# Performance work log

Hardware: AMD Instinct MI355X
Metric: run time of the kernel (lower is better)

Reference implementation:

```python
import jax, jax.numpy as jnp
import numpy as np

B, V, J, NS, NE = 2048, 5023, 5, 100, 50
PB = 9 * (J - 1)  # pose basis = 36


def setup_inputs() -> dict:
    key = jax.random.key(0)
    ks = jax.random.split(key, 8)
    jr = jax.random.uniform(ks[5], (J, V), dtype=jnp.float32)
    lw = jax.random.uniform(ks[6], (V, J), dtype=jnp.float32)
    return {
        "shape_params": jax.random.normal(ks[0], (B, NS), dtype=jnp.float32),
        "expression_params": jax.random.normal(ks[1], (B, NE), dtype=jnp.float32),
        "pose": jax.random.normal(ks[2], (B, J * 3), dtype=jnp.float32) * 0.2,
        "v_template": jax.random.normal(ks[3], (V, 3), dtype=jnp.float32) * 0.1,
        "shapedirs": jax.random.normal(ks[4], (V, 3, NS + NE), dtype=jnp.float32) * 0.01,
        "posedirs": jax.random.normal(ks[7], (PB, V * 3), dtype=jnp.float32) * 0.01,
        "J_regressor": jr / jnp.sum(jr, axis=1, keepdims=True),   # rows sum to 1 (convex combos)
        "lbs_weights": lw / jnp.sum(lw, axis=1, keepdims=True),   # rows sum to 1 (skinning weights)
        "parents": np.array([0, 0, 1, 1, 1], dtype=np.int64),     # FLAME kintree (root entry unused)
    }


def batch_rodrigues(rot_vecs):
    """(N,3) axis-angle -> (N,3,3) rotation matrices (matches torch ref incl. +1e-8)."""
    angle = jnp.linalg.norm(rot_vecs + 1e-8, axis=1, keepdims=True)      # (N,1)
    rd = rot_vecs / angle
    cos = jnp.cos(angle)[:, :, None]                                      # (N,1,1)
    sin = jnp.sin(angle)[:, :, None]
    rx, ry, rz = rd[:, 0], rd[:, 1], rd[:, 2]
    z = jnp.zeros_like(rx)
    K = jnp.stack([z, -rz, ry, rz, z, -rx, -ry, rx, z], axis=1).reshape(-1, 3, 3)
    I = jnp.eye(3, dtype=rot_vecs.dtype)
    return I + sin * K + (1.0 - cos) * jnp.matmul(K, K)


def reference(shape_params, expression_params, pose, v_template, shapedirs,
              posedirs, J_regressor, lbs_weights, parents):
    par = np.asarray(parents)  # static kinematic tree
    b = shape_params.shape[0]
    betas = jnp.concatenate([shape_params, expression_params], axis=1)     # (B,150)
    v_shaped = v_template + jnp.einsum('bl,vkl->bvk', betas, shapedirs)    # (B,V,3)
    Jts = jnp.einsum('bvk,jv->bjk', v_shaped, J_regressor)                 # (B,J,3)
    # pose -> rotations, pose-corrective offsets
    rot_mats = batch_rodrigues(pose.reshape(-1, 3)).reshape(b, -1, 3, 3)   # (B,J,3,3)
    I3 = jnp.eye(3, dtype=pose.dtype)
    pose_feature = (rot_mats[:, 1:] - I3).reshape(b, -1)                   # (B,36)
    pose_offsets = jnp.matmul(pose_feature, posedirs).reshape(b, -1, 3)    # (B,V,3)
    v_posed = v_posed = pose_offsets + v_shaped
    # kinematic chain (relative joint transforms -> world transforms)
    rel_joints = jnp.concatenate(
        [Jts[:, :1], Jts[:, 1:] - Jts[:, par[1:]]], axis=1)                # (B,J,3)
    top = jnp.concatenate([rot_mats, rel_joints[..., None]], axis=-1)      # (B,J,3,4)
    bottom = jnp.broadcast_to(
        jnp.array([0., 0., 0., 1.], dtype=pose.dtype), (b, Jts.shape[1], 1, 4))
    tm = jnp.concatenate([top, bottom], axis=2)                            # (B,J,4,4)
    chain = [tm[:, 0]]
    for i in range(1, par.shape[0]):  # tiny fixed loop over 5 joints
        chain.append(jnp.matmul(chain[int(par[i])], tm[:, i]))
    transforms = jnp.stack(chain, axis=1)                                  # (B,J,4,4)
    posed_joints = transforms[:, :, :3, 3]
    # remove rest-pose joint locations: subtract (transforms @ [j;0]) from last column
    tj = jnp.einsum('bjmn,bjn->bjm', transforms[:, :, :, :3], Jts)         # (B,J,4)
    rel_transforms = transforms.at[:, :, :, 3].add(-tj)                    # (B,J,4,4)
    # linear blend skinning
    T = jnp.einsum('vj,bjmn->bvmn', lbs_weights, rel_transforms)           # (B,V,4,4)
    verts = jnp.einsum('bvmn,bvn->bvm', T[:, :, :3, :3], v_posed) + T[:, :, :3, 3]
    return verts, posed_joints
```

## Files before the change

kernel.cpp:

```cpp
#include <hip/hip_runtime.h>
#include <hip/hip_bf16.h>
#include <math.h>

#define B_N 2048
#define V_N 5023
#define V3_N 15069
#define NSJB 157
#define CHUNK 32

typedef float f32x4 __attribute__((ext_vector_type(4)));
typedef short short8 __attribute__((ext_vector_type(8)));

static __device__ __forceinline__ ushort f2bf(float f) {
  __hip_bfloat16 h = __float2bfloat16(f);
  return *reinterpret_cast<ushort*>(&h);
}

__global__ void k_zero(float* __restrict__ SJ) {
  int id = blockIdx.x * 256 + threadIdx.x;
  if (id < 2280) SJ[id] = 0.0f;
}

__global__ __launch_bounds__(256) void k_pre(const float* __restrict__ sdirs,
                                             const float* __restrict__ pdirs,
                                             const float* __restrict__ vtemp,
                                             const float* __restrict__ Jr,
                                             const float* __restrict__ shp,
                                             const float* __restrict__ expr,
                                             ushort* __restrict__ basis,
                                             float* __restrict__ SJ,
                                             ushort* __restrict__ bb) {
  __shared__ float Sh[16][452];
  __shared__ float Pd[36][48];
  int t = threadIdx.x, blk = blockIdx.x;
  if (blk < 314) {
    int bx = blk, v0 = bx * 16;
    for (int idx = t; idx < 16 * 450; idx += 256) {
      int r = idx / 450, c = idx - r * 450;
      int v = v0 + r;
      Sh[r][c] = (v < V_N) ? sdirs[(size_t)v * 450 + c] : 0.0f;
    }
    for (int idx = t; idx < 36 * 48; idx += 256) {
      int p = idx / 48, c = idx - p * 48;
      int v3 = v0 * 3 + c;
      Pd[p][c] = (v3 < V3_N) ? pdirs[(size_t)p * V3_N + v3] : 0.0f;
    }
    __syncthreads();
    for (int idx = t; idx < 64 * 96; idx += 256) {
      int row = idx / 96, kp = idx - row * 96;
      int vl = row >> 2, c = row & 3;
      int k0 = kp * 2;
      float f0 = 0.0f, f1 = 0.0f;
      if (c < 3) {
        if (k0 < 150) {
          f0 = Sh[vl][c * 150 + k0];
          f1 = Sh[vl][c * 150 + k0 + 1];
        } else if (k0 < 186) {
          f0 = Pd[k0 - 150][vl * 3 + c];
          f1 = Pd[k0 - 149][vl * 3 + c];
        }
      }
      uint u = (uint)f2bf(f0) | ((uint)f2bf(f1) << 16);
      int kb = kp >> 2, e = kp & 3;
      ((uint*)basis)[(size_t)(bx * 64 + row) * 96 + (((kb ^ (row & 7)) << 2) + e)] = u;
    }
  } else if (blk < 314 + NSJB) {
    float (*JrL)[CHUNK] = (float(*)[CHUNK]) & Sh[0][0];
    int bk = blk - 314;
    int vstart = bk * CHUNK;
    int cnt = min(CHUNK, V_N - vstart);
    for (int idx = t; idx < 5 * CHUNK; idx += 256) {
      int j = idx / CHUNK, vi = idx % CHUNK;
      JrL[j][vi] = (vi < cnt) ? Jr[j * V_N + vstart + vi] : 0.0f;
    }
    __syncthreads();
    float acc0[5] = {0, 0, 0, 0, 0}, acc1[5] = {0, 0, 0, 0, 0};
    int c0 = t, c1 = t + 256;
#pragma unroll 4
    for (int vi = 0; vi < CHUNK; ++vi) {
      int v = min(vstart + vi, V_N - 1);
      float val0 = sdirs[(size_t)v * 450 + c0];
      float val1 = 0.0f;
      if (c1 < 450) val1 = sdirs[(size_t)v * 450 + c1];
      else if (c1 < 453) val1 = vtemp[(size_t)v * 3 + (c1 - 450)];
#pragma unroll
      for (int j = 0; j < 5; ++j) {
        float w = JrL[j][vi];
        acc0[j] = fmaf(w, val0, acc0[j]);
        acc1[j] = fmaf(w, val1, acc1[j]);
      }
    }
#pragma unroll
    for (int j = 0; j < 5; ++j) {
      atomicAdd(&SJ[j * 456 + c0], acc0[j]);
      if (c1 < 453) atomicAdd(&SJ[j * 456 + c1], acc1[j]);
    }
  } else {
    int idx = (blk - 314 - NSJB) * 256 + t;
    int b = idx / 96, cp = idx - b * 96;
    int c0 = cp * 2;
    float f0 = 0.0f, f1 = 0.0f;
    if (c0 < 100) {
      f0 = shp[(size_t)b * 100 + c0];
      f1 = shp[(size_t)b * 100 + c0 + 1];
    } else if (c0 < 150) {
      f0 = expr[(size_t)b * 50 + (c0 - 100)];
      f1 = expr[(size_t)b * 50 + (c0 - 99)];
    }
    int r = b & 63;
    int kb = cp >> 2, e = cp & 3;
    ((uint*)bb)[(size_t)b * 96 + (((kb ^ (r & 7)) << 2) + e)] =
        (uint)f2bf(f0) | ((uint)f2bf(f1) << 16);
  }
}

__global__ __launch_bounds__(256) void k_jpose(const float* __restrict__ shp,
                                               const float* __restrict__ expr,
                                               const float* __restrict__ SJ,
                                               const float* __restrict__ pose,
                                               ushort* __restrict__ bb,
                                               float* __restrict__ A,
                                               float* __restrict__ out) {
  __shared__ float JtL[16][16];
  int t = threadIdx.x;
  int g = t >> 4, r = t & 15;
  int b = blockIdx.x * 16 + g;
  if (r < 15) {
    int j = r / 3, k = r - j * 3;
    const float* SJr = SJ + j * 456;
    float acc = SJr[450 + k];
    const float* srow = shp + (size_t)b * 100;
    const float* erow = expr + (size_t)b * 50;
    for (int l = 0; l < 100; ++l) acc = fmaf(srow[l], SJr[k * 150 + l], acc);
    for (int l = 0; l < 50; ++l) acc = fmaf(erow[l], SJr[k * 150 + 100 + l], acc);
    JtL[g][r] = acc;
  }
  __syncthreads();
  if (r != 0) return;
  float R[5][3][3];
#pragma unroll
  for (int j = 0; j < 5; ++j) {
    float rx = pose[(size_t)b * 15 + j * 3 + 0];
    float ry = pose[(size_t)b * 15 + j * 3 + 1];
    float rz = pose[(size_t)b * 15 + j * 3 + 2];
    float sx = rx + 1e-8f, sy = ry + 1e-8f, sz = rz + 1e-8f;
    float ang = sqrtf(sx * sx + sy * sy + sz * sz);
    float inv = 1.0f / ang;
    float ux = rx * inv, uy = ry * inv, uz = rz * inv;
    float c = cosf(ang), s = sinf(ang), omc = 1.0f - c;
    float K[3][3] = {{0.0f, -uz, uy}, {uz, 0.0f, -ux}, {-uy, ux, 0.0f}};
#pragma unroll
    for (int m = 0; m < 3; ++m)
#pragma unroll
      for (int n = 0; n < 3; ++n) {
        float k2 = 0.0f;
#pragma unroll
        for (int q = 0; q < 3; ++q) k2 += K[m][q] * K[q][n];
        R[j][m][n] = ((m == n) ? 1.0f : 0.0f) + s * K[m][n] + omc * k2;
      }
  }
  {
    float pf[36];
#pragma unroll
    for (int j = 1; j < 5; ++j)
#pragma unroll
      for (int m = 0; m < 3; ++m)
#pragma unroll
        for (int n = 0; n < 3; ++n)
          pf[(j - 1) * 9 + m * 3 + n] = R[j][m][n] - ((m == n) ? 1.0f : 0.0f);
    uint* bbu = (uint*)bb + (size_t)b * 96;
    int rr = b & 7;
#pragma unroll
    for (int q = 0; q < 18; ++q) {
      int cp = 75 + q;
      int kb = cp >> 2, e = cp & 3;
      bbu[((kb ^ rr) << 2) + e] = (uint)f2bf(pf[2 * q]) | ((uint)f2bf(pf[2 * q + 1]) << 16);
    }
  }
  float Jt[5][3];
#pragma unroll
  for (int j = 0; j < 5; ++j)
#pragma unroll
    for (int k = 0; k < 3; ++k) Jt[j][k] = JtL[g][j * 3 + k];
  const int par[5] = {0, 0, 1, 1, 1};
  float rel[5][3];
#pragma unroll
  for (int k = 0; k < 3; ++k) rel[0][k] = Jt[0][k];
#pragma unroll
  for (int j = 1; j < 5; ++j)
#pragma unroll
    for (int k = 0; k < 3; ++k) rel[j][k] = Jt[j][k] - Jt[par[j]][k];
  float Rg[5][3][3], tg[5][3];
#pragma unroll
  for (int m = 0; m < 3; ++m) {
#pragma unroll
    for (int n = 0; n < 3; ++n) Rg[0][m][n] = R[0][m][n];
    tg[0][m] = rel[0][m];
  }
#pragma unroll
  for (int j = 1; j < 5; ++j) {
    int p = par[j];
#pragma unroll
    for (int m = 0; m < 3; ++m) {
      float t2 = tg[p][m];
#pragma unroll
      for (int n = 0; n < 3; ++n) {
        float s = 0.0f;
#pragma unroll
        for (int q = 0; q < 3; ++q) s = fmaf(Rg[p][m][q], R[j][q][n], s);
        Rg[j][m][n] = s;
        t2 = fmaf(Rg[p][m][n], rel[j][n], t2);
      }
      tg[j][m] = t2;
    }
  }
#pragma unroll
  for (int j = 0; j < 5; ++j)
#pragma unroll
    for (int k = 0; k < 3; ++k)
      out[(size_t)B_N * V_N * 3 + ((size_t)b * 5 + j) * 3 + k] = tg[j][k];
  float Af[5][12];
#pragma unroll
  for (int j = 0; j < 5; ++j)
#pragma unroll
    for (int m = 0; m < 3; ++m) {
      float tj = 0.0f;
#pragma unroll
      for (int n = 0; n < 3; ++n) {
        Af[j][m * 4 + n] = Rg[j][m][n];
        tj = fmaf(Rg[j][m][n], Jt[j][n], tj);
      }
      Af[j][m * 4 + 3] = tg[j][m] - tj;
    }
  float* Ab = A + (size_t)b * 64;
#pragma unroll
  for (int q = 0; q < 12; ++q) Ab[q] = Af[0][q];
#pragma unroll
  for (int j = 1; j < 5; ++j)
#pragma unroll
    for (int q = 0; q < 12; ++q) Ab[j * 12 + q] = Af[j][q] - Af[0][q];
}

__global__ __launch_bounds__(512, 6) void k_main(const ushort* __restrict__ basis,
                                                 const ushort* __restrict__ bb,
                                                 const float* __restrict__ Amat,
                                                 const float* __restrict__ lw,
                                                 const float* __restrict__ vtemp,
                                                 float* __restrict__ out) {
  __shared__ alignas(16) ushort AL[64 * 192];
  __shared__ alignas(16) ushort BL[64 * 192];
  float* AmL = (float*)AL;
  int t = threadIdx.x;
  int bx = blockIdx.y;
  int by = blockIdx.x;
  int b0 = by * 64;
  int lane = t & 63;
  int w = __builtin_amdgcn_readfirstlane(t >> 6);
  {
    const char* gA = (const char*)(basis + (size_t)bx * 64 * 192);
    const char* gB = (const char*)(bb + (size_t)b0 * 192);
#pragma unroll
    for (int i = 0; i < 3; ++i) {
      int chunk = w * 3 + i;
      int off = chunk * 1024 + lane * 16;
      __builtin_amdgcn_global_load_lds(
          (const __attribute__((address_space(1))) uint*)(gA + off),
          (__attribute__((address_space(3))) uint*)((char*)&AL[0] + chunk * 1024), 16, 0, 0);
      __builtin_amdgcn_global_load_lds(
          (const __attribute__((address_space(1))) uint*)(gB + off),
          (__attribute__((address_space(3))) uint*)((char*)&BL[0] + chunk * 1024), 16, 0, 0);
    }
  }
  __syncthreads();
  int wm = w >> 1, wn = w & 1;
  int lm = lane & 15, g = lane >> 4;
  f32x4 acc0 = {0.f, 0.f, 0.f, 0.f}, acc1 = {0.f, 0.f, 0.f, 0.f};
  const int ar = wm * 16 + lm;
  const int br0 = wn * 32 + lm;
  const int br1 = wn * 32 + 16 + lm;
#pragma unroll
  for (int ks = 0; ks < 6; ++ks) {
    int kb = ks * 4 + g;
    short8 af = *(const short8*)(&AL[(ar * 24 + (kb ^ (ar & 7))) * 8]);
    short8 bf0 = *(const short8*)(&BL[(br0 * 24 + (kb ^ (br0 & 7))) * 8]);
    short8 bf1 = *(const short8*)(&BL[(br1 * 24 + (kb ^ (br1 & 7))) * 8]);
    acc0 = __builtin_amdgcn_mfma_f32_16x16x32_bf16(af, bf0, acc0, 0, 0, 0);
    acc1 = __builtin_amdgcn_mfma_f32_16x16x32_bf16(af, bf1, acc1, 0, 0, 0);
  }
  int v = bx * 16 + wm * 4 + g;
  bool valid = v < V_N;
  int vv = valid ? v : 0;
  float wv[4];
#pragma unroll
  for (int j = 0; j < 4; ++j) wv[j] = lw[(size_t)vv * 5 + 1 + j];
  float vt0 = vtemp[(size_t)vv * 3 + 0];
  float vt1 = vtemp[(size_t)vv * 3 + 1];
  float vt2 = vtemp[(size_t)vv * 3 + 2];
  __syncthreads();
#pragma unroll
  for (int i = 0; i < 2; ++i) {
    int c = t + i * 512;
    int r = c / 16, q = (c % 16) * 4;
    *(f32x4*)(&AmL[r * 68 + q]) = *(const f32x4*)(&Amat[((size_t)(b0 + r)) * 64 + q]);
  }
  __syncthreads();
#pragma unroll
  for (int ni = 0; ni < 2; ++ni) {
    f32x4 p = ni ? acc1 : acc0;
    int bl = wn * 32 + ni * 16 + lm;
    const float* Ar = &AmL[bl * 68];
    f32x4 T0 = *(const f32x4*)(Ar + 0);
    f32x4 T1 = *(const f32x4*)(Ar + 4);
    f32x4 T2 = *(const f32x4*)(Ar + 8);
#pragma unroll
    for (int j = 1; j < 5; ++j) {
      f32x4 d0 = *(const f32x4*)(Ar + j * 12 + 0);
      f32x4 d1 = *(const f32x4*)(Ar + j * 12 + 4);
      f32x4 d2 = *(const f32x4*)(Ar + j * 12 + 8);
      float wjv = wv[j - 1];
#pragma unroll
      for (int c = 0; c < 4; ++c) {
        T0[c] = fmaf(wjv, d0[c], T0[c]);
        T1[c] = fmaf(wjv, d1[c], T1[c]);
        T2[c] = fmaf(wjv, d2[c], T2[c]);
      }
    }
    float x = p[0] + vt0, y = p[1] + vt1, z = p[2] + vt2;
    float ox = fmaf(T0[0], x, fmaf(T0[1], y, fmaf(T0[2], z, T0[3])));
    float oy = fmaf(T1[0], x, fmaf(T1[1], y, fmaf(T1[2], z, T1[3])));
    float oz = fmaf(T2[0], x, fmaf(T2[1], y, fmaf(T2[2], z, T2[3])));
    if (valid) {
      size_t o = ((size_t)(b0 + bl)) * V3_N + (size_t)v * 3;
      out[o + 0] = ox;
      out[o + 1] = oy;
      out[o + 2] = oz;
    }
  }
}

extern "C" void kernel_launch(void* const* d_in, const int* in_sizes, int n_in,
                              void* d_out, int out_size, void* d_ws, size_t ws_size,
                              hipStream_t stream) {
  const float* shp = (const float*)d_in[0];
  const float* expr = (const float*)d_in[1];
  const float* pose = (const float*)d_in[2];
  const float* vtemp = (const float*)d_in[3];
  const float* sdirs = (const float*)d_in[4];
  const float* pdirs = (const float*)d_in[5];
  const float* Jr = (const float*)d_in[6];
  const float* lw = (const float*)d_in[7];
  float* out = (float*)d_out;
  float* wsf = (float*)d_ws;

  const size_t OFF_SJ = 358400;
  const size_t OFF_A = 786688;
  const size_t OFF_BB = 917760;
  const size_t OFF_BASIS = 1114368;
  float* SJ = wsf + OFF_SJ;
  float* A = wsf + OFF_A;
  ushort* bb = (ushort*)(wsf + OFF_BB);
  ushort* basis = (ushort*)(wsf + OFF_BASIS);

  hipLaunchKernelGGL(k_zero, dim3(9), dim3(256), 0, stream, SJ);
  hipLaunchKernelGGL(k_pre, dim3(314 + NSJB + 768), dim3(256), 0, stream,
                     sdirs, pdirs, vtemp, Jr, shp, expr, basis, SJ, bb);
  hipLaunchKernelGGL(k_jpose, dim3(128), dim3(256), 0, stream,
                     shp, expr, SJ, pose, bb, A, out);
  hipLaunchKernelGGL(k_main, dim3(32, 314), dim3(512), 0, stream,
                     basis, bb, A, lw, vtemp, out);
}
```

Measured before the change: 108.3 us.

## Merge prologue kernels into one cooperative kernel with grid syncs

Merges the zero, preprocessing and joint/pose kernels into a single cooperative kernel that uses grid-wide syncs between phases and grid-stride loops over work units. This removes two kernel launches and their inter-kernel gaps before the main GEMM kernel. The trade-offs are the cost of the grid barriers, a grid capped at occupancy (per-CU count times 256), and fewer blocks running the jpose phase. The old three-kernel path remains as a fallback if the cooperative launch fails.

```diff
diff --git a/kernel.cpp b/kernel.cpp
--- a/kernel.cpp
+++ b/kernel.cpp
@@ -1,6 +1,9 @@
 #include <hip/hip_runtime.h>
+#include <hip/hip_cooperative_groups.h>
 #include <hip/hip_bf16.h>
 #include <math.h>
+
+namespace cg = cooperative_groups;
 
 #define B_N 2048
 #define V_N 5023
@@ -14,6 +17,259 @@
 static __device__ __forceinline__ ushort f2bf(float f) {
   __hip_bfloat16 h = __float2bfloat16(f);
   return *reinterpret_cast<ushort*>(&h);
+}
+
+
+static __device__ __forceinline__ void basis_unit(int bx, int t,
+                                                  const float* __restrict__ sdirs,
+                                                  const float* __restrict__ pdirs,
+                                                  ushort* __restrict__ basis) {
+  __shared__ float Sh[16][452];
+  __shared__ float Pd[36][48];
+  int v0 = bx * 16;
+  for (int idx = t; idx < 16 * 450; idx += 256) {
+    int r = idx / 450, c = idx - r * 450;
+    int v = v0 + r;
+    Sh[r][c] = (v < V_N) ? sdirs[(size_t)v * 450 + c] : 0.0f;
+  }
+  for (int idx = t; idx < 36 * 48; idx += 256) {
+    int p = idx / 48, c = idx - p * 48;
+    int v3 = v0 * 3 + c;
+    Pd[p][c] = (v3 < V3_N) ? pdirs[(size_t)p * V3_N + v3] : 0.0f;
+  }
+  __syncthreads();
+  for (int idx = t; idx < 64 * 96; idx += 256) {
+    int row = idx / 96, kp = idx - row * 96;
+    int vl = row >> 2, c = row & 3;
+    int k0 = kp * 2;
+    float f0 = 0.0f, f1 = 0.0f;
+    if (c < 3) {
+      if (k0 < 150) {
+        f0 = Sh[vl][c * 150 + k0];
+        f1 = Sh[vl][c * 150 + k0 + 1];
+      } else if (k0 < 186) {
+        f0 = Pd[k0 - 150][vl * 3 + c];
+        f1 = Pd[k0 - 149][vl * 3 + c];
+      }
+    }
+    uint u = (uint)f2bf(f0) | ((uint)f2bf(f1) << 16);
+    int kb = kp >> 2, e = kp & 3;
+    ((uint*)basis)[(size_t)(bx * 64 + row) * 96 + (((kb ^ (row & 7)) << 2) + e)] = u;
+  }
+  __syncthreads();
+}
+
+static __device__ __forceinline__ void sj_unit(int bk, int t,
+                                               const float* __restrict__ sdirs,
+                                               const float* __restrict__ vtemp,
+                                               const float* __restrict__ Jr,
+                                               float* __restrict__ SJ) {
+  __shared__ float JrL[5][CHUNK];
+  int vstart = bk * CHUNK;
+  int cnt = min(CHUNK, V_N - vstart);
+  for (int idx = t; idx < 5 * CHUNK; idx += 256) {
+    int j = idx / CHUNK, vi = idx % CHUNK;
+    JrL[j][vi] = (vi < cnt) ? Jr[j * V_N + vstart + vi] : 0.0f;
+  }
+  __syncthreads();
+  float acc0[5] = {0, 0, 0, 0, 0}, acc1[5] = {0, 0, 0, 0, 0};
+  int c0 = t, c1 = t + 256;
+#pragma unroll 4
+  for (int vi = 0; vi < CHUNK; ++vi) {
+    int v = min(vstart + vi, V_N - 1);
+    float val0 = sdirs[(size_t)v * 450 + c0];
+    float val1 = 0.0f;
+    if (c1 < 450) val1 = sdirs[(size_t)v * 450 + c1];
+    else if (c1 < 453) val1 = vtemp[(size_t)v * 3 + (c1 - 450)];
+#pragma unroll
+    for (int j = 0; j < 5; ++j) {
+      float w = JrL[j][vi];
+      acc0[j] = fmaf(w, val0, acc0[j]);
+      acc1[j] = fmaf(w, val1, acc1[j]);
+    }
+  }
+#pragma unroll
+  for (int j = 0; j < 5; ++j) {
+    atomicAdd(&SJ[j * 456 + c0], acc0[j]);
+    if (c1 < 453) atomicAdd(&SJ[j * 456 + c1], acc1[j]);
+  }
+  __syncthreads();
+}
+
+static __device__ __forceinline__ void bext_unit(int chunk, int t,
+                                                 const float* __restrict__ shp,
+                                                 const float* __restrict__ expr,
+                                                 ushort* __restrict__ bb) {
+  int idx = chunk * 256 + t;
+  int b = idx / 96, cp = idx - b * 96;
+  int c0 = cp * 2;
+  float f0 = 0.0f, f1 = 0.0f;
+  if (c0 < 100) {
+    f0 = shp[(size_t)b * 100 + c0];
+    f1 = shp[(size_t)b * 100 + c0 + 1];
+  } else if (c0 < 150) {
+    f0 = expr[(size_t)b * 50 + (c0 - 100)];
+    f1 = expr[(size_t)b * 50 + (c0 - 99)];
+  }
+  int r = b & 63;
+  int kb = cp >> 2, e = cp & 3;
+  ((uint*)bb)[(size_t)b * 96 + (((kb ^ (r & 7)) << 2) + e)] =
+      (uint)f2bf(f0) | ((uint)f2bf(f1) << 16);
+}
+
+static __device__ __forceinline__ void jpose_unit(int u, int t,
+                                                  const float* __restrict__ shp,
+                                                  const float* __restrict__ expr,
+                                                  const float* __restrict__ SJ,
+                                                  const float* __restrict__ pose,
+                                                  ushort* __restrict__ bb,
+                                                  float* __restrict__ A,
+                                                  float* __restrict__ out) {
+  __shared__ float JtL[16][16];
+  int g = t >> 4, r = t & 15;
+  int b = u * 16 + g;
+  if (r < 15) {
+    int j = r / 3, k = r - j * 3;
+    const float* SJr = SJ + j * 456;
+    float acc = SJr[450 + k];
+    const float* srow = shp + (size_t)b * 100;
+    const float* erow = expr + (size_t)b * 50;
+    for (int l = 0; l < 100; ++l) acc = fmaf(srow[l], SJr[k * 150 + l], acc);
+    for (int l = 0; l < 50; ++l) acc = fmaf(erow[l], SJr[k * 150 + 100 + l], acc);
+    JtL[g][r] = acc;
+  }
+  __syncthreads();
+  if (r == 0) {
+    float R[5][3][3];
+#pragma unroll
+    for (int j = 0; j < 5; ++j) {
+      float rx = pose[(size_t)b * 15 + j * 3 + 0];
+      float ry = pose[(size_t)b * 15 + j * 3 + 1];
+      float rz = pose[(size_t)b * 15 + j * 3 + 2];
+      float sx = rx + 1e-8f, sy = ry + 1e-8f, sz = rz + 1e-8f;
+      float ang = sqrtf(sx * sx + sy * sy + sz * sz);
+      float inv = 1.0f / ang;
+      float ux = rx * inv, uy = ry * inv, uz = rz * inv;
+      float c = cosf(ang), s = sinf(ang), omc = 1.0f - c;
+      float K[3][3] = {{0.0f, -uz, uy}, {uz, 0.0f, -ux}, {-uy, ux, 0.0f}};
+#pragma unroll
+      for (int m = 0; m < 3; ++m)
+#pragma unroll
+        for (int n = 0; n < 3; ++n) {
+          float k2 = 0.0f;
+#pragma unroll
+          for (int q = 0; q < 3; ++q) k2 += K[m][q] * K[q][n];
+          R[j][m][n] = ((m == n) ? 1.0f : 0.0f) + s * K[m][n] + omc * k2;
+        }
+    }
+    {
+      float pf[36];
+#pragma unroll
+      for (int j = 1; j < 5; ++j)
+#pragma unroll
+        for (int m = 0; m < 3; ++m)
+#pragma unroll
+          for (int n = 0; n < 3; ++n)
+            pf[(j - 1) * 9 + m * 3 + n] = R[j][m][n] - ((m == n) ? 1.0f : 0.0f);
+      uint* bbu = (uint*)bb + (size_t)b * 96;
+      int rr = b & 7;
+#pragma unroll
+      for (int q = 0; q < 18; ++q) {
+        int cp = 75 + q;
+        int kb = cp >> 2, e = cp & 3;
+        bbu[((kb ^ rr) << 2) + e] = (uint)f2bf(pf[2 * q]) | ((uint)f2bf(pf[2 * q + 1]) << 16);
+      }
+    }
+    float Jt[5][3];
+#pragma unroll
+    for (int j = 0; j < 5; ++j)
+#pragma unroll
+      for (int k = 0; k < 3; ++k) Jt[j][k] = JtL[g][j * 3 + k];
+    const int par[5] = {0, 0, 1, 1, 1};
+    float rel[5][3];
+#pragma unroll
+    for (int k = 0; k < 3; ++k) rel[0][k] = Jt[0][k];
+#pragma unroll
+    for (int j = 1; j < 5; ++j)
+#pragma unroll
+      for (int k = 0; k < 3; ++k) rel[j][k] = Jt[j][k] - Jt[par[j]][k];
+    float Rg[5][3][3], tg[5][3];
+#pragma unroll
+    for (int m = 0; m < 3; ++m) {
+#pragma unroll
+      for (int n = 0; n < 3; ++n) Rg[0][m][n] = R[0][m][n];
+      tg[0][m] = rel[0][m];
+    }
+#pragma unroll
+    for (int j = 1; j < 5; ++j) {
+      int p = par[j];
+#pragma unroll
+      for (int m = 0; m < 3; ++m) {
+        float t2 = tg[p][m];
+#pragma unroll
+        for (int n = 0; n < 3; ++n) {
+          float s = 0.0f;
+#pragma unroll
+          for (int q = 0; q < 3; ++q) s = fmaf(Rg[p][m][q], R[j][q][n], s);
+          Rg[j][m][n] = s;
+          t2 = fmaf(Rg[p][m][n], rel[j][n], t2);
+        }
+        tg[j][m] = t2;
+      }
+    }
+#pragma unroll
+    for (int j = 0; j < 5; ++j)
+#pragma unroll
+      for (int k = 0; k < 3; ++k)
+        out[(size_t)B_N * V_N * 3 + ((size_t)b * 5 + j) * 3 + k] = tg[j][k];
+    float Af[5][12];
+#pragma unroll
+    for (int j = 0; j < 5; ++j)
+#pragma unroll
+      for (int m = 0; m < 3; ++m) {
+        float tj = 0.0f;
+#pragma unroll
+        for (int n = 0; n < 3; ++n) {
+          Af[j][m * 4 + n] = Rg[j][m][n];
+          tj = fmaf(Rg[j][m][n], Jt[j][n], tj);
+        }
+        Af[j][m * 4 + 3] = tg[j][m] - tj;
+      }
+    float* Ab = A + (size_t)b * 64;
+#pragma unroll
+    for (int q = 0; q < 12; ++q) Ab[q] = Af[0][q];
+#pragma unroll
+    for (int j = 1; j < 5; ++j)
+#pragma unroll
+      for (int q = 0; q < 12; ++q) Ab[j * 12 + q] = Af[j][q] - Af[0][q];
+  }
+  __syncthreads();
+}
+
+__global__ __launch_bounds__(256) void k_prologue(const float* __restrict__ sdirs,
+                                                  const float* __restrict__ pdirs,
+                                                  const float* __restrict__ vtemp,
+                                                  const float* __restrict__ Jr,
+                                                  const float* __restrict__ shp,
+                                                  const float* __restrict__ expr,
+                                                  const float* __restrict__ pose,
+                                                  ushort* __restrict__ basis,
+                                                  float* __restrict__ SJ,
+                                                  ushort* __restrict__ bb,
+                                                  float* __restrict__ A,
+                                                  float* __restrict__ out) {
+  cg::grid_group grid = cg::this_grid();
+  int t = threadIdx.x;
+  for (int id = blockIdx.x * 256 + t; id < 2280; id += gridDim.x * 256) SJ[id] = 0.0f;
+  grid.sync();
+  for (int u = blockIdx.x; u < 314 + NSJB + 768; u += gridDim.x) {
+    if (u < 314) basis_unit(u, t, sdirs, pdirs, basis);
+    else if (u < 314 + NSJB) sj_unit(u - 314, t, sdirs, vtemp, Jr, SJ);
+    else bext_unit(u - 314 - NSJB, t, shp, expr, bb);
+  }
+  grid.sync();
+  for (int u = blockIdx.x; u < 128; u += gridDim.x)
+    jpose_unit(u, t, shp, expr, SJ, pose, bb, A, out);
 }
 
 __global__ void k_zero(float* __restrict__ SJ) {
@@ -30,88 +286,10 @@
                                              ushort* __restrict__ basis,
                                              float* __restrict__ SJ,
                                              ushort* __restrict__ bb) {
-  __shared__ float Sh[16][452];
-  __shared__ float Pd[36][48];
-  int t = threadIdx.x, blk = blockIdx.x;
-  if (blk < 314) {
-    int bx = blk, v0 = bx * 16;
-    for (int idx = t; idx < 16 * 450; idx += 256) {
-      int r = idx / 450, c = idx - r * 450;
-      int v = v0 + r;
-      Sh[r][c] = (v < V_N) ? sdirs[(size_t)v * 450 + c] : 0.0f;
-    }
-    for (int idx = t; idx < 36 * 48; idx += 256) {
-      int p = idx / 48, c = idx - p * 48;
-      int v3 = v0 * 3 + c;
-      Pd[p][c] = (v3 < V3_N) ? pdirs[(size_t)p * V3_N + v3] : 0.0f;
-    }
-    __syncthreads();
-    for (int idx = t; idx < 64 * 96; idx += 256) {
-      int row = idx / 96, kp = idx - row * 96;
-      int vl = row >> 2, c = row & 3;
-      int k0 = kp * 2;
-      float f0 = 0.0f, f1 = 0.0f;
-      if (c < 3) {
-        if (k0 < 150) {
-          f0 = Sh[vl][c * 150 + k0];
-          f1 = Sh[vl][c * 150 + k0 + 1];
-        } else if (k0 < 186) {
-          f0 = Pd[k0 - 150][vl * 3 + c];
-          f1 = Pd[k0 - 149][vl * 3 + c];
-        }
-      }
-      uint u = (uint)f2bf(f0) | ((uint)f2bf(f1) << 16);
-      int kb = kp >> 2, e = kp & 3;
-      ((uint*)basis)[(size_t)(bx * 64 + row) * 96 + (((kb ^ (row & 7)) << 2) + e)] = u;
-    }
-  } else if (blk < 314 + NSJB) {
-    float (*JrL)[CHUNK] = (float(*)[CHUNK]) & Sh[0][0];
-    int bk = blk - 314;
-    int vstart = bk * CHUNK;
-    int cnt = min(CHUNK, V_N - vstart);
-    for (int idx = t; idx < 5 * CHUNK; idx += 256) {
-      int j = idx / CHUNK, vi = idx % CHUNK;
-      JrL[j][vi] = (vi < cnt) ? Jr[j * V_N + vstart + vi] : 0.0f;
-    }
-    __syncthreads();
-    float acc0[5] = {0, 0, 0, 0, 0}, acc1[5] = {0, 0, 0, 0, 0};
-    int c0 = t, c1 = t + 256;
-#pragma unroll 4
-    for (int vi = 0; vi < CHUNK; ++vi) {
-      int v = min(vstart + vi, V_N - 1);
-      float val0 = sdirs[(size_t)v * 450 + c0];
-      float val1 = 0.0f;
-      if (c1 < 450) val1 = sdirs[(size_t)v * 450 + c1];
-      else if (c1 < 453) val1 = vtemp[(size_t)v * 3 + (c1 - 450)];
-#pragma unroll
-      for (int j = 0; j < 5; ++j) {
-        float w = JrL[j][vi];
-        acc0[j] = fmaf(w, val0, acc0[j]);
-        acc1[j] = fmaf(w, val1, acc1[j]);
-      }
-    }
-#pragma unroll
-    for (int j = 0; j < 5; ++j) {
-      atomicAdd(&SJ[j * 456 + c0], acc0[j]);
-      if (c1 < 453) atomicAdd(&SJ[j * 456 + c1], acc1[j]);
-    }
-  } else {
-    int idx = (blk - 314 - NSJB) * 256 + t;
-    int b = idx / 96, cp = idx - b * 96;
-    int c0 = cp * 2;
-    float f0 = 0.0f, f1 = 0.0f;
-    if (c0 < 100) {
-      f0 = shp[(size_t)b * 100 + c0];
-      f1 = shp[(size_t)b * 100 + c0 + 1];
-    } else if (c0 < 150) {
-      f0 = expr[(size_t)b * 50 + (c0 - 100)];
-      f1 = expr[(size_t)b * 50 + (c0 - 99)];
-    }
-    int r = b & 63;
-    int kb = cp >> 2, e = cp & 3;
-    ((uint*)bb)[(size_t)b * 96 + (((kb ^ (r & 7)) << 2) + e)] =
-        (uint)f2bf(f0) | ((uint)f2bf(f1) << 16);
-  }
+  int blk = blockIdx.x, t = threadIdx.x;
+  if (blk < 314) basis_unit(blk, t, sdirs, pdirs, basis);
+  else if (blk < 314 + NSJB) sj_unit(blk - 314, t, sdirs, vtemp, Jr, SJ);
+  else bext_unit(blk - 314 - NSJB, t, shp, expr, bb);
 }
 
 __global__ __launch_bounds__(256) void k_jpose(const float* __restrict__ shp,
@@ -121,124 +299,7 @@
                                                ushort* __restrict__ bb,
                                                float* __restrict__ A,
                                                float* __restrict__ out) {
-  __shared__ float JtL[16][16];
-  int t = threadIdx.x;
-  int g = t >> 4, r = t & 15;
-  int b = blockIdx.x * 16 + g;
-  if (r < 15) {
-    int j = r / 3, k = r - j * 3;
-    const float* SJr = SJ + j * 456;
-    float acc = SJr[450 + k];
-    const float* srow = shp + (size_t)b * 100;
-    const float* erow = expr + (size_t)b * 50;
-    for (int l = 0; l < 100; ++l) acc = fmaf(srow[l], SJr[k * 150 + l], acc);
-    for (int l = 0; l < 50; ++l) acc = fmaf(erow[l], SJr[k * 150 + 100 + l], acc);
-    JtL[g][r] = acc;
-  }
-  __syncthreads();
-  if (r != 0) return;
-  float R[5][3][3];
-#pragma unroll
-  for (int j = 0; j < 5; ++j) {
-    float rx = pose[(size_t)b * 15 + j * 3 + 0];
-    float ry = pose[(size_t)b * 15 + j * 3 + 1];
-    float rz = pose[(size_t)b * 15 + j * 3 + 2];
-    float sx = rx + 1e-8f, sy = ry + 1e-8f, sz = rz + 1e-8f;
-    float ang = sqrtf(sx * sx + sy * sy + sz * sz);
-    float inv = 1.0f / ang;
-    float ux = rx * inv, uy = ry * inv, uz = rz * inv;
-    float c = cosf(ang), s = sinf(ang), omc = 1.0f - c;
-    float K[3][3] = {{0.0f, -uz, uy}, {uz, 0.0f, -ux}, {-uy, ux, 0.0f}};
-#pragma unroll
-    for (int m = 0; m < 3; ++m)
-#pragma unroll
-      for (int n = 0; n < 3; ++n) {
-        float k2 = 0.0f;
-#pragma unroll
-        for (int q = 0; q < 3; ++q) k2 += K[m][q] * K[q][n];
-        R[j][m][n] = ((m == n) ? 1.0f : 0.0f) + s * K[m][n] + omc * k2;
-      }
-  }
-  {
-    float pf[36];
-#pragma unroll
-    for (int j = 1; j < 5; ++j)
-#pragma unroll
-      for (int m = 0; m < 3; ++m)
-#pragma unroll
-        for (int n = 0; n < 3; ++n)
-          pf[(j - 1) * 9 + m * 3 + n] = R[j][m][n] - ((m == n) ? 1.0f : 0.0f);
-    uint* bbu = (uint*)bb + (size_t)b * 96;
-    int rr = b & 7;
-#pragma unroll
-    for (int q = 0; q < 18; ++q) {
-      int cp = 75 + q;
-      int kb = cp >> 2, e = cp & 3;
-      bbu[((kb ^ rr) << 2) + e] = (uint)f2bf(pf[2 * q]) | ((uint)f2bf(pf[2 * q + 1]) << 16);
-    }
-  }
-  float Jt[5][3];
-#pragma unroll
-  for (int j = 0; j < 5; ++j)
-#pragma unroll
-    for (int k = 0; k < 3; ++k) Jt[j][k] = JtL[g][j * 3 + k];
-  const int par[5] = {0, 0, 1, 1, 1};
-  float rel[5][3];
-#pragma unroll
-  for (int k = 0; k < 3; ++k) rel[0][k] = Jt[0][k];
-#pragma unroll
-  for (int j = 1; j < 5; ++j)
-#pragma unroll
-    for (int k = 0; k < 3; ++k) rel[j][k] = Jt[j][k] - Jt[par[j]][k];
-  float Rg[5][3][3], tg[5][3];
-#pragma unroll
-  for (int m = 0; m < 3; ++m) {
-#pragma unroll
-    for (int n = 0; n < 3; ++n) Rg[0][m][n] = R[0][m][n];
-    tg[0][m] = rel[0][m];
-  }
-#pragma unroll
-  for (int j = 1; j < 5; ++j) {
-    int p = par[j];
-#pragma unroll
-    for (int m = 0; m < 3; ++m) {
-      float t2 = tg[p][m];
-#pragma unroll
-      for (int n = 0; n < 3; ++n) {
-        float s = 0.0f;
-#pragma unroll
-        for (int q = 0; q < 3; ++q) s = fmaf(Rg[p][m][q], R[j][q][n], s);
-        Rg[j][m][n] = s;
-        t2 = fmaf(Rg[p][m][n], rel[j][n], t2);
-      }
-      tg[j][m] = t2;
-    }
-  }
-#pragma unroll
-  for (int j = 0; j < 5; ++j)
-#pragma unroll
-    for (int k = 0; k < 3; ++k)
-      out[(size_t)B_N * V_N * 3 + ((size_t)b * 5 + j) * 3 + k] = tg[j][k];
-  float Af[5][12];
-#pragma unroll
-  for (int j = 0; j < 5; ++j)
-#pragma unroll
-    for (int m = 0; m < 3; ++m) {
-      float tj = 0.0f;
-#pragma unroll
-      for (int n = 0; n < 3; ++n) {
-        Af[j][m * 4 + n] = Rg[j][m][n];
-        tj = fmaf(Rg[j][m][n], Jt[j][n], tj);
-      }
-      Af[j][m * 4 + 3] = tg[j][m] - tj;
-    }
-  float* Ab = A + (size_t)b * 64;
-#pragma unroll
-  for (int q = 0; q < 12; ++q) Ab[q] = Af[0][q];
-#pragma unroll
-  for (int j = 1; j < 5; ++j)
-#pragma unroll
-    for (int q = 0; q < 12; ++q) Ab[j * 12 + q] = Af[j][q] - Af[0][q];
+  jpose_unit(blockIdx.x, threadIdx.x, shp, expr, SJ, pose, bb, A, out);
 }
 
 __global__ __launch_bounds__(512, 6) void k_main(const ushort* __restrict__ basis,
@@ -361,11 +422,33 @@
   ushort* bb = (ushort*)(wsf + OFF_BB);
   ushort* basis = (ushort*)(wsf + OFF_BASIS);
 
-  hipLaunchKernelGGL(k_zero, dim3(9), dim3(256), 0, stream, SJ);
-  hipLaunchKernelGGL(k_pre, dim3(314 + NSJB + 768), dim3(256), 0, stream,
-                     sdirs, pdirs, vtemp, Jr, shp, expr, basis, SJ, bb);
-  hipLaunchKernelGGL(k_jpose, dim3(128), dim3(256), 0, stream,
-                     shp, expr, SJ, pose, bb, A, out);
+  int maxB = 0;
+  hipError_t qe = hipOccupancyMaxActiveBlocksPerMultiprocessor(&maxB, k_prologue, 256, 0);
+  int coopGrid = 512;
+  if (qe == hipSuccess && maxB > 0) {
+    long cap = (long)maxB * 256;
+    coopGrid = (int)(cap < 1239 ? cap : 1239);
+  }
+
+  const float* sdirs_c = sdirs;
+  const float* pdirs_c = pdirs;
+  const float* vtemp_c = vtemp;
+  const float* Jr_c = Jr;
+  const float* shp_c = shp;
+  const float* expr_c = expr;
+  const float* pose_c = pose;
+  void* kargs[] = {(void*)&sdirs_c, (void*)&pdirs_c, (void*)&vtemp_c, (void*)&Jr_c,
+                   (void*)&shp_c,   (void*)&expr_c,  (void*)&pose_c,  (void*)&basis,
+                   (void*)&SJ,      (void*)&bb,      (void*)&A,       (void*)&out};
+  hipError_t ce = hipLaunchCooperativeKernel((void*)k_prologue, dim3(coopGrid), dim3(256),
+                                             kargs, 0, stream);
+  if (ce != hipSuccess) {
+    hipLaunchKernelGGL(k_zero, dim3(9), dim3(256), 0, stream, SJ);
+    hipLaunchKernelGGL(k_pre, dim3(314 + NSJB + 768), dim3(256), 0, stream,
+                       sdirs, pdirs, vtemp, Jr, shp, expr, basis, SJ, bb);
+    hipLaunchKernelGGL(k_jpose, dim3(128), dim3(256), 0, stream,
+                       shp, expr, SJ, pose, bb, A, out);
+  }
   hipLaunchKernelGGL(k_main, dim3(32, 314), dim3(512), 0, stream,
                      basis, bb, A, lw, vtemp, out);
 }
```

New measurement: 171.2 us. 1.58x slower.
